# Kernel tuning notes

Hardware: AMD Instinct MI355X
Metric: run time of the kernel (lower is better)

The kernel has to match this reference:

```python
import jax, jax.numpy as jnp
import numpy as np

N_NODES = 10000
N_EDGES = 160000
EMBED = 512
RBF = 64
ANG = 16


def setup_inputs() -> dict:
    key = jax.random.key(0)
    ks = jax.random.split(key, 12)
    x = jax.random.normal(ks[0], (N_NODES, EMBED), dtype=jnp.float32)
    coord = jax.random.normal(ks[1], (N_NODES, 3), dtype=jnp.float32)
    edge_index = jax.random.randint(ks[2], (2, N_EDGES), 0, N_NODES, dtype=jnp.int64)
    rbf_feature = jax.random.normal(ks[3], (N_EDGES, RBF), dtype=jnp.float32)
    angle_feature = jax.random.normal(ks[4], (N_EDGES, ANG), dtype=jnp.float32)
    s = 1.0 / np.sqrt(RBF + ANG)
    W_edge = jax.random.normal(ks[5], (RBF + ANG, EMBED), dtype=jnp.float32) * s
    b_edge = jax.random.normal(ks[6], (EMBED,), dtype=jnp.float32) * 0.01
    s2 = 1.0 / np.sqrt(EMBED)
    W1 = jax.random.normal(ks[7], (EMBED, EMBED), dtype=jnp.float32) * s2
    b1 = jax.random.normal(ks[8], (EMBED,), dtype=jnp.float32) * 0.01
    W2 = jax.random.normal(ks[9], (EMBED, EMBED), dtype=jnp.float32) * s2
    b2 = jax.random.normal(ks[10], (EMBED,), dtype=jnp.float32) * 0.01
    return {"x": x, "coord": coord, "edge_index": edge_index,
            "rbf_feature": rbf_feature, "angle_feature": angle_feature,
            "W_edge": W_edge, "b_edge": b_edge,
            "W1": W1, "b1": b1, "W2": W2, "b2": b2}


def reference(x, coord, edge_index, rbf_feature, angle_feature,
              W_edge, b_edge, W1, b1, W2, b2):
    row = edge_index[0]  # destination nodes for scatter-add
    edge_feat = jnp.concatenate([rbf_feature, angle_feature], axis=-1)  # [E, 80]
    msg = edge_feat @ W_edge + b_edge                                    # [E, D]
    agg = jax.ops.segment_sum(msg, row, num_segments=x.shape[0])         # [N, D]
    h = jax.nn.relu(agg @ W1 + b1) @ W2 + b2                             # node MLP
    return x + h
```

## Files before the change

### kernel.cpp

```cpp
#include <hip/hip_runtime.h>

constexpr int NN = 10000;
constexpr int NE = 160000;
constexpr int D  = 512;
constexpr int KC = 8;
constexpr int MAXDEG = 96;

typedef __attribute__((ext_vector_type(8))) short short8;
typedef __attribute__((ext_vector_type(4))) float f32x4;

static __device__ __forceinline__ ushort f2bf(float f) {
    union { float f; unsigned u; } v; v.f = f;
    unsigned r = (v.u + 0x7FFFu + ((v.u >> 16) & 1u)) >> 16;
    return (ushort)r;
}

typedef __attribute__((address_space(3))) unsigned int lds_uint;
typedef const __attribute__((address_space(1))) unsigned int glb_uint;
static __device__ __forceinline__ void gload16(const ushort* g, ushort* l) {
    __builtin_amdgcn_global_load_lds((glb_uint*)g, (lds_uint*)l, 16, 0, 0);
}

__global__ __launch_bounds__(256)
void prep1_kernel(const float* __restrict__ We,
                  const float* __restrict__ be,
                  const float* __restrict__ W1,
                  const float* __restrict__ W2,
                  float* __restrict__ part,
                  ushort* __restrict__ W2t,
                  int* __restrict__ deg) {
    __shared__ float tile[32][33];
    const int b   = blockIdx.x;
    const int tid = threadIdx.x;

    if (b < 1344) {
        const int c  = (b & 7) * 64 + (tid & 63);
        const int r  = ((b >> 3) % 21) * 4 + (tid >> 6);
        const int kc = b / 168;
        if (r > 80) return;
        const float* arow = (r < 80) ? (We + (size_t)r * D) : be;
        const int k0 = kc * 64;
        float s = 0.f;
        #pragma unroll
        for (int k = 0; k < 64; k += 4) {
            float4 a = *reinterpret_cast<const float4*>(&arow[k0 + k]);
            s += a.x * W1[(size_t)(k0 + k    ) * D + c];
            s += a.y * W1[(size_t)(k0 + k + 1) * D + c];
            s += a.z * W1[(size_t)(k0 + k + 2) * D + c];
            s += a.w * W1[(size_t)(k0 + k + 3) * D + c];
        }
        part[((size_t)kc * 81 + r) * D + c] = s;
    } else if (b < 1600) {
        const int t  = b - 1344;
        const int bx = (t & 15) * 32;
        const int by = (t >> 4) * 32;
        const int tx = tid & 31;
        const int ty = tid >> 5;
        #pragma unroll
        for (int i = 0; i < 4; ++i)
            tile[ty + 8 * i][tx] = W2[(size_t)(by + ty + 8 * i) * D + bx + tx];
        __syncthreads();
        #pragma unroll
        for (int i = 0; i < 4; ++i)
            W2t[(size_t)(bx + ty + 8 * i) * D + by + tx] = f2bf(tile[tx][ty + 8 * i]);
    } else {
        const int i = (b - 1600) * 256 + tid;
        if (i < NN) deg[i] = 0;
    }
}

__global__ __launch_bounds__(256)
void prep2_kernel(const float* __restrict__ part,
                  const int* __restrict__ row,
                  ushort* __restrict__ WcT,
                  int* __restrict__ deg,
                  int* __restrict__ ell) {
    const int b   = blockIdx.x;
    const int tid = threadIdx.x;
    if (b < 256) {
        const int i = b * 256 + tid;
        const int k = i >> 9;
        const int c = i & 511;
        float s = 0.f;
        if (k <= 80) {
            #pragma unroll
            for (int kc = 0; kc < KC; ++kc)
                s += part[((size_t)kc * 81 + k) * D + c];
        }
        WcT[(size_t)c * 128 + k] = f2bf(s);
    } else {
        const int e = (b - 256) * 256 + tid;
        if (e < NE) {
            int r = row[e];
            int slot = atomicAdd(&deg[r], 1);
            if (slot < MAXDEG) ell[r * MAXDEG + slot] = e;
        }
    }
}

__global__ __launch_bounds__(256)
void gather_agg_kernel(const int* __restrict__ deg,
                       const int* __restrict__ ell,
                       const float* __restrict__ rbf,
                       const float* __restrict__ ang,
                       ushort* __restrict__ aggX) {
    const int wv   = threadIdx.x >> 6;
    const int lane = threadIdx.x & 63;
    const int n    = blockIdx.x * 4 + wv;
    if (n >= NN) return;
    int d = deg[n];
    if (d > MAXDEG) d = MAXDEG;
    const int* en = ell + (size_t)n * MAXDEG;
    float s1 = 0.f, s2 = 0.f;
    int i = 0;
    for (; i + 4 <= d; i += 4) {
        const int e0 = en[i], e1 = en[i + 1], e2 = en[i + 2], e3 = en[i + 3];
        const float v0 = rbf[e0 * 64 + lane];
        const float v1 = rbf[e1 * 64 + lane];
        const float v2 = rbf[e2 * 64 + lane];
        const float v3 = rbf[e3 * 64 + lane];
        if (lane < 16) {
            s2 += ang[e0 * 16 + lane] + ang[e1 * 16 + lane]
                + ang[e2 * 16 + lane] + ang[e3 * 16 + lane];
        }
        s1 += v0 + v1 + v2 + v3;
    }
    for (; i < d; ++i) {
        const int e = en[i];
        s1 += rbf[e * 64 + lane];
        if (lane < 16) s2 += ang[e * 16 + lane];
    }
    aggX[(size_t)n * 128 + lane] = f2bf(s1);
    const float v2 = (lane < 16) ? s2 : (lane == 16 ? (float)d : 0.f);
    aggX[(size_t)n * 128 + 64 + lane] = f2bf(v2);
}

__global__ __launch_bounds__(256)
void h1_mfma_kernel(const ushort* __restrict__ A,
                    const ushort* __restrict__ Bt,
                    const float* __restrict__ b1,
                    ushort* __restrict__ H, int M) {
    __shared__ ushort As[64 * 128];
    __shared__ ushort Bs[64 * 128];
    const int tid  = threadIdx.x;
    const int lane = tid & 63;
    const int wid  = tid >> 6;
    const int wm   = wid >> 1;
    const int wn   = wid & 1;

    const int l = blockIdx.y * gridDim.x + blockIdx.x;
    const int cpx = (gridDim.x * gridDim.y) >> 3;
    const int t_ = (l & 7) * cpx + (l >> 3);
    const int n0 = (t_ & 7) * 64;
    const int m0 = (t_ >> 3) * 64;

    const int r0 = tid >> 4;
    const int ch = tid & 15;

    f32x4 acc[2][2] = {};

    #pragma unroll
    for (int j = 0; j < 4; ++j) {
        const int r  = j * 16 + r0;
        const int cs = (ch ^ (r & 7)) * 8;
        const int rowbase = j * 16 + wid * 4;
        gload16(A  + (size_t)(m0 + r) * 128 + cs, &As[rowbase * 128]);
        gload16(Bt + (size_t)(n0 + r) * 128 + cs, &Bs[rowbase * 128]);
    }
    __syncthreads();

    #pragma unroll
    for (int kk = 0; kk < 4; ++kk) {
        const int kc = kk * 4 + (lane >> 4);
        short8 af[2], bfr[2];
        #pragma unroll
        for (int mf = 0; mf < 2; ++mf) {
            const int ar = wm * 32 + mf * 16 + (lane & 15);
            af[mf] = *reinterpret_cast<const short8*>(
                &As[ar * 128 + ((kc ^ (ar & 7)) * 8)]);
        }
        #pragma unroll
        for (int nf = 0; nf < 2; ++nf) {
            const int br = wn * 32 + nf * 16 + (lane & 15);
            bfr[nf] = *reinterpret_cast<const short8*>(
                &Bs[br * 128 + ((kc ^ (br & 7)) * 8)]);
        }
        #pragma unroll
        for (int mf = 0; mf < 2; ++mf)
            #pragma unroll
            for (int nf = 0; nf < 2; ++nf)
                acc[mf][nf] = __builtin_amdgcn_mfma_f32_16x16x32_bf16(
                    af[mf], bfr[nf], acc[mf][nf], 0, 0, 0);
    }

    #pragma unroll
    for (int mf = 0; mf < 2; ++mf) {
        const int rowb = m0 + wm * 32 + mf * 16 + ((lane >> 4) << 2);
        #pragma unroll
        for (int nf = 0; nf < 2; ++nf) {
            const int col = n0 + wn * 32 + nf * 16 + (lane & 15);
            const float bv = b1[col];
            #pragma unroll
            for (int r = 0; r < 4; ++r) {
                const int row = rowb + r;
                if (row < M)
                    H[(size_t)row * D + col] = f2bf(fmaxf(acc[mf][nf][r] + bv, 0.f));
            }
        }
    }
}

__global__ __launch_bounds__(256)
void mfma_gemm_kernel(const ushort* __restrict__ A,
                      const ushort* __restrict__ Bt,
                      const float* __restrict__ bias,
                      const float* __restrict__ xres,
                      float* __restrict__ Cout, int M) {
    __shared__ ushort As[2][64 * 64];
    __shared__ ushort Bs[2][64 * 64];
    const int tid  = threadIdx.x;
    const int lane = tid & 63;
    const int wid  = tid >> 6;
    const int wm   = wid >> 1;
    const int wn   = wid & 1;

    const int l = blockIdx.y * gridDim.x + blockIdx.x;
    const int cpx = (gridDim.x * gridDim.y) >> 3;
    const int t_ = (l & 7) * cpx + (l >> 3);
    const int n0 = (t_ & 7) * 64;
    const int m0 = (t_ >> 3) * 64;

    const int sr = lane >> 3;
    const int sc = lane & 7;

    f32x4 acc[2][2] = {};
    constexpr int KTILES = D / 64;

    auto stage = [&](int buf, int t) {
        #pragma unroll
        for (int j = 0; j < 2; ++j) {
            const int r  = wid * 16 + j * 8 + sr;
            const int cs = (sc ^ (r & 7)) * 8;
            const int rowbase = wid * 16 + j * 8;
            gload16(A  + (size_t)(m0 + r) * D + t * 64 + cs, &As[buf][rowbase * 64]);
            gload16(Bt + (size_t)(n0 + r) * D + t * 64 + cs, &Bs[buf][rowbase * 64]);
        }
    };

    stage(0, 0);
    __syncthreads();

    for (int t = 0; t < KTILES; ++t) {
        const int cur = t & 1;
        if (t + 1 < KTILES) stage(cur ^ 1, t + 1);
        #pragma unroll
        for (int kk = 0; kk < 2; ++kk) {
            const int kc = kk * 4 + (lane >> 4);
            short8 af[2], bfr[2];
            #pragma unroll
            for (int mf = 0; mf < 2; ++mf) {
                const int ar = wm * 32 + mf * 16 + (lane & 15);
                af[mf] = *reinterpret_cast<const short8*>(
                    &As[cur][ar * 64 + ((kc ^ (ar & 7)) * 8)]);
            }
            #pragma unroll
            for (int nf = 0; nf < 2; ++nf) {
                const int br = wn * 32 + nf * 16 + (lane & 15);
                bfr[nf] = *reinterpret_cast<const short8*>(
                    &Bs[cur][br * 64 + ((kc ^ (br & 7)) * 8)]);
            }
            #pragma unroll
            for (int mf = 0; mf < 2; ++mf)
                #pragma unroll
                for (int nf = 0; nf < 2; ++nf)
                    acc[mf][nf] = __builtin_amdgcn_mfma_f32_16x16x32_bf16(
                        af[mf], bfr[nf], acc[mf][nf], 0, 0, 0);
        }
        __syncthreads();
    }

    #pragma unroll
    for (int mf = 0; mf < 2; ++mf) {
        const int rowb = m0 + wm * 32 + mf * 16 + ((lane >> 4) << 2);
        #pragma unroll
        for (int nf = 0; nf < 2; ++nf) {
            const int col = n0 + wn * 32 + nf * 16 + (lane & 15);
            const float bv = bias[col];
            #pragma unroll
            for (int r = 0; r < 4; ++r) {
                const int row = rowb + r;
                if (row < M)
                    Cout[(size_t)row * D + col] =
                        acc[mf][nf][r] + bv + xres[(size_t)row * D + col];
            }
        }
    }
}

extern "C" void kernel_launch(void* const* d_in, const int* in_sizes, int n_in,
                              void* d_out, int out_size, void* d_ws, size_t ws_size,
                              hipStream_t stream) {
    const float* x      = (const float*)d_in[0];
    const int*   edge_index = (const int*)d_in[2];
    const float* rbf    = (const float*)d_in[3];
    const float* ang    = (const float*)d_in[4];
    const float* W_edge = (const float*)d_in[5];
    const float* b_edge = (const float*)d_in[6];
    const float* W1     = (const float*)d_in[7];
    const float* b1     = (const float*)d_in[8];
    const float* W2     = (const float*)d_in[9];
    const float* b2     = (const float*)d_in[10];
    float* out = (float*)d_out;

    char* w = (char*)d_ws;
    ushort* aggX = (ushort*)w;
    ushort* W2t  = (ushort*)(w + 2560000);
    ushort* WcT  = (ushort*)(w + 3084288);
    int*    deg  = (int*)(w + 3215360);
    float*  part = (float*)(w + 3255360);
    int*    ell  = (int*)(w + 4582464);
    ushort* h1   = (ushort*)(w + 3255360);

    prep1_kernel<<<1640, 256, 0, stream>>>(W_edge, b_edge, W1, W2, part, W2t, deg);
    prep2_kernel<<<881, 256, 0, stream>>>(part, edge_index, WcT, deg, ell);
    gather_agg_kernel<<<NN / 4, 256, 0, stream>>>(deg, ell, rbf, ang, aggX);

    dim3 ggrid(D / 64, (NN + 63) / 64);
    h1_mfma_kernel<<<ggrid, 256, 0, stream>>>(aggX, WcT, b1, h1, NN);
    mfma_gemm_kernel<<<ggrid, 256, 0, stream>>>(h1, W2t, b2, x, out, NN);
}
```

Baseline: 75.45 us.

## Enlarge GEMM M-tile to 128 rows and unroll gather loop by eight

```diff
diff --git a/kernel.cpp b/kernel.cpp
--- a/kernel.cpp
+++ b/kernel.cpp
@@ -113,6 +113,20 @@
     const int* en = ell + (size_t)n * MAXDEG;
     float s1 = 0.f, s2 = 0.f;
     int i = 0;
+    for (; i + 8 <= d; i += 8) {
+        int e[8];
+        #pragma unroll
+        for (int j = 0; j < 8; ++j) e[j] = en[i + j];
+        float v[8];
+        #pragma unroll
+        for (int j = 0; j < 8; ++j) v[j] = rbf[e[j] * 64 + lane];
+        if (lane < 16) {
+            #pragma unroll
+            for (int j = 0; j < 8; ++j) s2 += ang[e[j] * 16 + lane];
+        }
+        #pragma unroll
+        for (int j = 0; j < 8; ++j) s1 += v[j];
+    }
     for (; i + 4 <= d; i += 4) {
         const int e0 = en[i], e1 = en[i + 1], e2 = en[i + 2], e3 = en[i + 3];
         const float v0 = rbf[e0 * 64 + lane];
@@ -140,31 +154,36 @@
                     const ushort* __restrict__ Bt,
                     const float* __restrict__ b1,
                     ushort* __restrict__ H, int M) {
-    __shared__ ushort As[64 * 128];
+    __shared__ ushort As[128 * 128];
     __shared__ ushort Bs[64 * 128];
     const int tid  = threadIdx.x;
     const int lane = tid & 63;
     const int wid  = tid >> 6;
-    const int wm   = wid >> 1;
-    const int wn   = wid & 1;
 
     const int l = blockIdx.y * gridDim.x + blockIdx.x;
     const int cpx = (gridDim.x * gridDim.y) >> 3;
     const int t_ = (l & 7) * cpx + (l >> 3);
     const int n0 = (t_ & 7) * 64;
-    const int m0 = (t_ >> 3) * 64;
-
-    const int r0 = tid >> 4;
-    const int ch = tid & 15;
-
-    f32x4 acc[2][2] = {};
-
+    const int m0 = (t_ >> 3) * 128;
+
+    const int rg = lane >> 4;
+    const int ch = lane & 15;
+
+    f32x4 acc[2][4] = {};
+
+    #pragma unroll
+    for (int j = 0; j < 8; ++j) {
+        const int r  = wid * 32 + j * 4 + rg;
+        const int gm = (m0 + r < M) ? (m0 + r) : (M - 1);
+        const int cs = (ch ^ (r & 7)) * 8;
+        const int rowbase = wid * 32 + j * 4;
+        gload16(A + (size_t)gm * 128 + cs, &As[rowbase * 128]);
+    }
     #pragma unroll
     for (int j = 0; j < 4; ++j) {
-        const int r  = j * 16 + r0;
+        const int r  = wid * 16 + j * 4 + rg;
         const int cs = (ch ^ (r & 7)) * 8;
-        const int rowbase = j * 16 + wid * 4;
-        gload16(A  + (size_t)(m0 + r) * 128 + cs, &As[rowbase * 128]);
+        const int rowbase = wid * 16 + j * 4;
         gload16(Bt + (size_t)(n0 + r) * 128 + cs, &Bs[rowbase * 128]);
     }
     __syncthreads();
@@ -172,33 +191,33 @@
     #pragma unroll
     for (int kk = 0; kk < 4; ++kk) {
         const int kc = kk * 4 + (lane >> 4);
-        short8 af[2], bfr[2];
+        short8 af[2], bfr[4];
         #pragma unroll
         for (int mf = 0; mf < 2; ++mf) {
-            const int ar = wm * 32 + mf * 16 + (lane & 15);
+            const int ar = wid * 32 + mf * 16 + (lane & 15);
             af[mf] = *reinterpret_cast<const short8*>(
                 &As[ar * 128 + ((kc ^ (ar & 7)) * 8)]);
         }
         #pragma unroll
-        for (int nf = 0; nf < 2; ++nf) {
-            const int br = wn * 32 + nf * 16 + (lane & 15);
+        for (int nf = 0; nf < 4; ++nf) {
+            const int br = nf * 16 + (lane & 15);
             bfr[nf] = *reinterpret_cast<const short8*>(
                 &Bs[br * 128 + ((kc ^ (br & 7)) * 8)]);
         }
         #pragma unroll
         for (int mf = 0; mf < 2; ++mf)
             #pragma unroll
-            for (int nf = 0; nf < 2; ++nf)
+            for (int nf = 0; nf < 4; ++nf)
                 acc[mf][nf] = __builtin_amdgcn_mfma_f32_16x16x32_bf16(
                     af[mf], bfr[nf], acc[mf][nf], 0, 0, 0);
     }
 
     #pragma unroll
     for (int mf = 0; mf < 2; ++mf) {
-        const int rowb = m0 + wm * 32 + mf * 16 + ((lane >> 4) << 2);
-        #pragma unroll
-        for (int nf = 0; nf < 2; ++nf) {
-            const int col = n0 + wn * 32 + nf * 16 + (lane & 15);
+        const int rowb = m0 + wid * 32 + mf * 16 + ((lane >> 4) << 2);
+        #pragma unroll
+        for (int nf = 0; nf < 4; ++nf) {
+            const int col = n0 + nf * 16 + (lane & 15);
             const float bv = b1[col];
             #pragma unroll
             for (int r = 0; r < 4; ++r) {
@@ -216,33 +235,38 @@
                       const float* __restrict__ bias,
                       const float* __restrict__ xres,
                       float* __restrict__ Cout, int M) {
-    __shared__ ushort As[2][64 * 64];
+    __shared__ ushort As[2][128 * 64];
     __shared__ ushort Bs[2][64 * 64];
     const int tid  = threadIdx.x;
     const int lane = tid & 63;
     const int wid  = tid >> 6;
-    const int wm   = wid >> 1;
-    const int wn   = wid & 1;
 
     const int l = blockIdx.y * gridDim.x + blockIdx.x;
     const int cpx = (gridDim.x * gridDim.y) >> 3;
     const int t_ = (l & 7) * cpx + (l >> 3);
     const int n0 = (t_ & 7) * 64;
-    const int m0 = (t_ >> 3) * 64;
+    const int m0 = (t_ >> 3) * 128;
 
     const int sr = lane >> 3;
     const int sc = lane & 7;
 
-    f32x4 acc[2][2] = {};
+    f32x4 acc[2][4] = {};
     constexpr int KTILES = D / 64;
 
     auto stage = [&](int buf, int t) {
+        #pragma unroll
+        for (int j = 0; j < 4; ++j) {
+            const int r  = wid * 32 + j * 8 + sr;
+            const int gm = (m0 + r < M) ? (m0 + r) : (M - 1);
+            const int cs = (sc ^ (r & 7)) * 8;
+            const int rowbase = wid * 32 + j * 8;
+            gload16(A + (size_t)gm * D + t * 64 + cs, &As[buf][rowbase * 64]);
+        }
         #pragma unroll
         for (int j = 0; j < 2; ++j) {
             const int r  = wid * 16 + j * 8 + sr;
             const int cs = (sc ^ (r & 7)) * 8;
             const int rowbase = wid * 16 + j * 8;
-            gload16(A  + (size_t)(m0 + r) * D + t * 64 + cs, &As[buf][rowbase * 64]);
             gload16(Bt + (size_t)(n0 + r) * D + t * 64 + cs, &Bs[buf][rowbase * 64]);
         }
     };
@@ -256,23 +280,23 @@
         #pragma unroll
         for (int kk = 0; kk < 2; ++kk) {
             const int kc = kk * 4 + (lane >> 4);
-            short8 af[2], bfr[2];
+            short8 af[2], bfr[4];
             #pragma unroll
             for (int mf = 0; mf < 2; ++mf) {
-                const int ar = wm * 32 + mf * 16 + (lane & 15);
+                const int ar = wid * 32 + mf * 16 + (lane & 15);
                 af[mf] = *reinterpret_cast<const short8*>(
                     &As[cur][ar * 64 + ((kc ^ (ar & 7)) * 8)]);
             }
             #pragma unroll
-            for (int nf = 0; nf < 2; ++nf) {
-                const int br = wn * 32 + nf * 16 + (lane & 15);
+            for (int nf = 0; nf < 4; ++nf) {
+                const int br = nf * 16 + (lane & 15);
                 bfr[nf] = *reinterpret_cast<const short8*>(
                     &Bs[cur][br * 64 + ((kc ^ (br & 7)) * 8)]);
             }
             #pragma unroll
             for (int mf = 0; mf < 2; ++mf)
                 #pragma unroll
-                for (int nf = 0; nf < 2; ++nf)
+                for (int nf = 0; nf < 4; ++nf)
                     acc[mf][nf] = __builtin_amdgcn_mfma_f32_16x16x32_bf16(
                         af[mf], bfr[nf], acc[mf][nf], 0, 0, 0);
         }
@@ -281,10 +305,10 @@
 
     #pragma unroll
     for (int mf = 0; mf < 2; ++mf) {
-        const int rowb = m0 + wm * 32 + mf * 16 + ((lane >> 4) << 2);
-        #pragma unroll
-        for (int nf = 0; nf < 2; ++nf) {
-            const int col = n0 + wn * 32 + nf * 16 + (lane & 15);
+        const int rowb = m0 + wid * 32 + mf * 16 + ((lane >> 4) << 2);
+        #pragma unroll
+        for (int nf = 0; nf < 4; ++nf) {
+            const int col = n0 + nf * 16 + (lane & 15);
             const float bv = bias[col];
             #pragma unroll
             for (int r = 0; r < 4; ++r) {
@@ -325,7 +349,7 @@
     prep2_kernel<<<881, 256, 0, stream>>>(part, edge_index, WcT, deg, ell);
     gather_agg_kernel<<<NN / 4, 256, 0, stream>>>(deg, ell, rbf, ang, aggX);
 
-    dim3 ggrid(D / 64, (NN + 63) / 64);
+    dim3 ggrid(D / 64, (NN + 127) / 128);
     h1_mfma_kernel<<<ggrid, 256, 0, stream>>>(aggX, WcT, b1, h1, NN);
     mfma_gemm_kernel<<<ggrid, 256, 0, stream>>>(h1, W2t, b2, x, out, NN);
 }
```

New measurement: 70.58 us. 6.5% less time.
